# Kernel optimization log

Measured on AMD Instinct MI355X. Metric: run time of the kernel, lower is better.

## Reference

```python
import jax, jax.numpy as jnp
import numpy as np

D_MODEL = 512
D_K = 64
D_V = 128
H = D_MODEL // D_V  # 4 heads (num_head = d_model // d_v per the source)
B, N = 4, 2048


def setup_inputs() -> dict:
    key = jax.random.key(0)
    k0, k1, k2, k3, k4 = jax.random.split(key, 5)
    s = 0.02
    return {
        "input_x": jax.random.normal(k0, (B, N, D_MODEL), jnp.float32),
        "Wq": jax.random.normal(k1, (D_MODEL, H * D_K), jnp.float32) * s,
        "Wk": jax.random.normal(k2, (D_MODEL, H * D_K), jnp.float32) * s,
        "Wv": jax.random.normal(k3, (D_MODEL, D_MODEL), jnp.float32) * s,
        "Wo": jax.random.normal(k4, (D_MODEL, D_MODEL), jnp.float32) * s,
    }


def reference(input_x, Wq, Wk, Wv, Wo):
    b, n, _ = input_x.shape
    # Contiguous per-head slices in the source == a simple reshape here.
    q = (input_x @ Wq).reshape(b, n, H, D_K)   # [B,N,H,dk]
    k = (input_x @ Wk).reshape(b, n, H, D_K)   # [B,N,H,dk]
    v = (input_x @ Wv).reshape(b, n, H, D_V)   # [B,N,H,dv]
    scale = jnp.sqrt(jnp.float32(D_K))
    scores = jnp.einsum('bqhd,bkhd->bhqk', q, k) / scale  # [B,H,N,N]
    # FAITHFUL quirk: the source uses nn.Softmax() with no dim on a 3D
    # (B,N,N) tensor; PyTorch's legacy dim inference picks dim=0 (batch).
    attn = jax.nn.softmax(scores, axis=0)
    out = jnp.einsum('bhqk,bkhd->bqhd', attn, v).reshape(b, n, H * D_V)
    return out @ Wo
```

## Files before the change

kernel.cpp:

```cpp
#include <hip/hip_runtime.h>
#include <hip/hip_bf16.h>


typedef __attribute__((ext_vector_type(8))) short short8;
typedef __attribute__((ext_vector_type(4))) float floatx4;
typedef unsigned short u16;
typedef unsigned int u32;

#define MFMA16(a, b, c) __builtin_amdgcn_mfma_f32_16x16x32_bf16((a), (b), (c), 0, 0, 0)

__device__ __forceinline__ u16 f2bf(float f) {
    union { float f; unsigned u; } v; v.f = f;
    unsigned r = v.u + 0x7fffu + ((v.u >> 16) & 1u);
    return (u16)(r >> 16);
}

__device__ __forceinline__ float bf2f(u16 b) {
    union { unsigned u; float f; } v; v.u = ((u32)b) << 16;
    return v.f;
}

__device__ __forceinline__ u32 pk2bf(float a, float b) {
#if __has_builtin(__builtin_amdgcn_cvt_pk_bf16_f32)
    typedef __attribute__((ext_vector_type(2))) __bf16 bf16x2;
    union { bf16x2 v; u32 u; } c;
    c.v = __builtin_amdgcn_cvt_pk_bf16_f32(a, b);
    return c.u;
#else
    return (u32)f2bf(a) | ((u32)f2bf(b) << 16);
#endif
}

__device__ __forceinline__ float ex2(float x) {
#if __has_builtin(__builtin_amdgcn_exp2f)
    return __builtin_amdgcn_exp2f(x);
#else
    return exp2f(x);
#endif
}

__device__ __forceinline__ void gload_lds16(const u16* g, u16* l) {
    __builtin_amdgcn_global_load_lds(
        (const __attribute__((address_space(1))) void*)(const void*)g,
        (__attribute__((address_space(3))) void*)(void*)l, 16, 0, 0);
}

__global__ __launch_bounds__(256) void prep_all_kernel(
    const float* __restrict__ x, u16* __restrict__ xb,
    const float* __restrict__ Wq, const float* __restrict__ Wk,
    const float* __restrict__ Wv, const float* __restrict__ Wo,
    u16* __restrict__ WallT, u16* __restrict__ WoT) {
    int bid = blockIdx.x;
    if (bid < 4096) {
        int i = bid * 256 + threadIdx.x;
        float4 v = ((const float4*)x)[i];
        ushort4 o;
        o.x = f2bf(v.x); o.y = f2bf(v.y); o.z = f2bf(v.z); o.w = f2bf(v.w);
        ((ushort4*)xb)[i] = o;
        return;
    }
    int i = (bid - 4096) * 256 + threadIdx.x;
    if (i < 524288) {
        int n = i >> 9, k = i & 511;
        float v;
        if (n < 256)      v = Wq[k * 256 + n] * 0.18033688011f;
        else if (n < 512) v = Wk[k * 256 + (n - 256)];
        else              v = Wv[k * 512 + (n - 512)];
        WallT[i] = f2bf(v);
    } else {
        int j = i - 524288;
        int n = j >> 9, k = j & 511;
        WoT[j] = f2bf(Wo[k * 512 + n]);
    }
}

__global__ __launch_bounds__(512) void gemm_qkv_kernel(
    const u16* __restrict__ A, const u16* __restrict__ BT,
    u16* __restrict__ Qp, u16* __restrict__ Kp, u16* __restrict__ Vp,
    int Kdim) {
    __shared__ u16 sm[16896];
    u16* Asl = sm;
    u16* Bsl = sm + 8192;
    const int tid = threadIdx.x;
    const int bid0 = blockIdx.y * 8 + blockIdx.x;
    const int xcd = bid0 & 7, jj = bid0 >> 3;
    const int mbase = (xcd * 8 + (jj >> 3)) * 128;
    const int nbase = (jj & 7) * 128;
    const int wave = tid >> 6, lane = tid & 63;
    const int wm = wave >> 2, wn = wave & 3;
    const int lq = lane & 15, quad = lane >> 4;

    const u16* gA = A + (size_t)(mbase + wave * 16 + (lane >> 3)) * Kdim + (lane & 7) * 8;
    const u16* gB = BT + (size_t)(nbase + wave * 16 + (lane >> 3)) * Kdim + (lane & 7) * 8;
    u16* lA = &Asl[(wave * 16) * 64];
    u16* lB = &Bsl[(wave * 16) * 64];

    const floatx4 z4 = {0.f, 0.f, 0.f, 0.f};
    floatx4 acc[4][2];
#pragma unroll
    for (int i = 0; i < 4; i++)
#pragma unroll
        for (int j = 0; j < 2; j++) acc[i][j] = z4;

    const int nk = Kdim >> 6;
    for (int kk = 0; kk < nk; kk++) {
        const int kb = kk << 6;
        if (kk) __syncthreads();
#pragma unroll
        for (int i = 0; i < 2; i++) {
            gload_lds16(gA + kb + (size_t)(i * 8) * Kdim, lA + (i * 8) * 64);
            gload_lds16(gB + kb + (size_t)(i * 8) * Kdim, lB + (i * 8) * 64);
        }
        __syncthreads();
#pragma unroll
        for (int ki = 0; ki < 2; ki++) {
            short8 af[4], bf[2];
#pragma unroll
            for (int mi = 0; mi < 4; mi++)
                af[mi] = *(const short8*)&Asl[(wm * 64 + mi * 16 + lq) * 64 + ki * 32 + quad * 8];
#pragma unroll
            for (int ni = 0; ni < 2; ni++)
                bf[ni] = *(const short8*)&Bsl[(wn * 32 + ni * 16 + lq) * 64 + ki * 32 + quad * 8];
#pragma unroll
            for (int mi = 0; mi < 4; mi++)
#pragma unroll
                for (int ni = 0; ni < 2; ni++)
                    acc[mi][ni] = MFMA16(af[mi], bf[ni], acc[mi][ni]);
        }
    }
    __syncthreads();
    const bool vtile = (nbase >= 512);
#pragma unroll
    for (int mi = 0; mi < 4; mi++)
#pragma unroll
        for (int ni = 0; ni < 2; ni++) {
            int cl = wn * 32 + ni * 16 + lq;
#pragma unroll
            for (int r = 0; r < 4; r++) {
                int rl = wm * 64 + mi * 16 + quad * 4 + r;
                if (vtile) sm[cl * 132 + rl] = f2bf(acc[mi][ni][r]);
                else       sm[rl * 132 + cl] = f2bf(acc[mi][ni][r]);
            }
        }
    __syncthreads();
    const int b = mbase >> 11;
    const int keyb = mbase & 2047;
    if (nbase < 256) {
        const int hq = nbase >> 6;
        const int qs_base = keyb >> 4;
#pragma unroll
        for (int t = 0; t < 4; t++) {
            int l = wave * 4 + t;
            int qs2 = l >> 2, h2 = (l >> 1) & 1, ki = l & 1;
            int qd = lane >> 4, lqq = lane & 15;
            short8 v = *(const short8*)&sm[(qs2 * 16 + lqq) * 132 + h2 * 64 + ki * 32 + qd * 8];
            int h = hq + h2;
            size_t base = ((size_t)(((b * 4 + h) * 128 + (qs_base + qs2)) * 2 + ki) * 64 + lane) << 3;
            *(short8*)&Qp[base] = v;
        }
    } else if (nbase < 512) {
        const int hb = (nbase - 256) >> 6;
        const int ktb = keyb >> 6;
#pragma unroll
        for (int t = 0; t < 4; t++) {
            int l = wave * 4 + t;
            int kt2 = l >> 4, hf = (l >> 3) & 1, nj = (l >> 2) & 1;
            int h2 = (l >> 1) & 1, ki = l & 1;
            int quadk = lane >> 4, lqk = lane & 15;
            short8 v = *(const short8*)&sm[(kt2 * 64 + hf * 32 + lqk * 2 + nj) * 132 +
                                           h2 * 64 + ki * 32 + quadk * 8];
            int h = hb + h2;
            size_t base = ((size_t)(((((b * 4 + h) * 32 + (ktb + kt2)) * 2 + hf) * 2 + nj)
                                    * 2 + ki) * 64 + lane) << 3;
            *(short8*)&Kp[base] = v;
        }
    } else {
        const int h = (nbase - 512) >> 7;
        const int ktb = keyb >> 6;
#pragma unroll
        for (int t = 0; t < 4; t++) {
            int l = wave * 4 + t;
            int kt2 = l >> 4, hf = (l >> 3) & 1, niv = (l >> 1) & 3, wv = l & 1;
            int quadv = lane >> 4, lqv = lane & 15;
            short8 v = *(const short8*)&sm[(hf * 64 + niv * 16 + lqv) * 132 +
                                           kt2 * 64 + wv * 32 + quadv * 8];
            size_t base = ((size_t)(((((b * 4 + h) * 32 + (ktb + kt2)) * 2 + hf) * 4 + niv)
                                    * 2 + wv) * 64 + lane) << 3;
            *(short8*)&Vp[base] = v;
        }
    }
}

__global__ __launch_bounds__(512) void gemm_out_kernel(
    const u16* __restrict__ A, const u16* __restrict__ BT,
    float* __restrict__ Cf, int Kdim, int ldc) {
    __shared__ u16 Asl[64 * 64];
    __shared__ u16 Bsl[128 * 64];
    const int tid = threadIdx.x;
    const int bid0 = blockIdx.y * 4 + blockIdx.x;
    const int xcd = bid0 & 7, jj = bid0 >> 3;
    const int mbase = (xcd * 16 + (jj >> 2)) * 64;
    const int nbase = (jj & 3) * 128;
    const int wave = tid >> 6, lane = tid & 63;
    const int wm = wave >> 2, wn = wave & 3;
    const int lq = lane & 15, quad = lane >> 4;
    const size_t S = (size_t)8192 * 512;

    const u16* gA = A + (size_t)(mbase + wave * 8 + (lane >> 3)) * Kdim + (lane & 7) * 8;
    const u16* gB = BT + (size_t)(nbase + wave * 16 + (lane >> 3)) * Kdim + (lane & 7) * 8;
    u16* lAw = &Asl[(wave * 8 + (lane >> 3)) * 64 + (lane & 7) * 8];
    u16* lB = &Bsl[(wave * 16) * 64];

    const floatx4 z4 = {0.f, 0.f, 0.f, 0.f};
    floatx4 acc[2][2];
#pragma unroll
    for (int i = 0; i < 2; i++)
#pragma unroll
        for (int j = 0; j < 2; j++) acc[i][j] = z4;

    const int nk = Kdim >> 6;
    for (int kk = 0; kk < nk; kk++) {
        const int kb = kk << 6;
        short8 p0 = *(const short8*)(gA + kb);
        short8 p1 = *(const short8*)(gA + kb + S);
        short8 p2 = *(const short8*)(gA + kb + 2 * S);
        short8 p3 = *(const short8*)(gA + kb + 3 * S);
        if (kk) __syncthreads();
        gload_lds16(gB + kb, lB);
        gload_lds16(gB + kb + (size_t)8 * Kdim, lB + 8 * 64);
        short8 o;
#pragma unroll
        for (int j2 = 0; j2 < 8; j2++) {
            float s = bf2f((u16)p0[j2]) + bf2f((u16)p1[j2]) +
                      bf2f((u16)p2[j2]) + bf2f((u16)p3[j2]);
            o[j2] = (short)f2bf(s);
        }
        *(short8*)lAw = o;
        __syncthreads();
#pragma unroll
        for (int ki = 0; ki < 2; ki++) {
            short8 af[2], bf[2];
#pragma unroll
            for (int mi = 0; mi < 2; mi++)
                af[mi] = *(const short8*)&Asl[(wm * 32 + mi * 16 + lq) * 64 + ki * 32 + quad * 8];
#pragma unroll
            for (int ni = 0; ni < 2; ni++)
                bf[ni] = *(const short8*)&Bsl[(wn * 32 + ni * 16 + lq) * 64 + ki * 32 + quad * 8];
#pragma unroll
            for (int mi = 0; mi < 2; mi++)
#pragma unroll
                for (int ni = 0; ni < 2; ni++)
                    acc[mi][ni] = MFMA16(af[mi], bf[ni], acc[mi][ni]);
        }
    }
#pragma unroll
    for (int mi = 0; mi < 2; mi++)
#pragma unroll
        for (int ni = 0; ni < 2; ni++)
#pragma unroll
            for (int r = 0; r < 4; r++)
                Cf[(size_t)(mbase + wm * 32 + mi * 16 + quad * 4 + r) * ldc +
                   (nbase + wn * 32 + ni * 16 + lq)] = acc[mi][ni][r];
}

__global__ __launch_bounds__(512) void attn_kernel(const u16* __restrict__ Qp,
                                                   const u16* __restrict__ Kp,
                                                   const u16* __restrict__ Vp,
                                                   u16* __restrict__ Pp) {
    __shared__ u16 pl[2 * 4 * 4096];
    const int bx = blockIdx.x;
    const int xcd = bx & 7;
    const int j8 = bx >> 3;
    const int sl = xcd * 2 + (j8 >> 5);
    const int h = sl & 3;
    const int ck = sl >> 2;
    const int qt = j8 & 31;
    const int tid = threadIdx.x;
    const int wave = tid >> 6, lane = tid & 63;
    const int mi = wave & 3, half = wave >> 2;
    const int dq = wave;
    const int half_v = dq >> 2, ni_v = dq & 3;
    const int lq = lane & 15, quad = lane >> 4;
    const int qs = qt * 4 + mi;

    short8 aq[4][2];
#pragma unroll
    for (int b = 0; b < 4; b++)
#pragma unroll
        for (int ki = 0; ki < 2; ki++)
            aq[b][ki] = *(const short8*)&Qp[
                ((size_t)((((b * 4 + h) * 128 + qs) * 2 + ki) * 64 + lane) << 3)];

    const floatx4 z4 = {0.f, 0.f, 0.f, 0.f};
    floatx4 oacc[4][4];
#pragma unroll
    for (int b = 0; b < 4; b++)
#pragma unroll
        for (int m2 = 0; m2 < 4; m2++) oacc[b][m2] = z4;

    for (int kt = ck * 8; kt < ck * 8 + 8; kt++) {
        u16* plb = &pl[((kt & 1) * 4 + mi) * 4096];
        u16* plbuf = &pl[(kt & 1) * 4 * 4096];
        floatx4 s[4][2];
        __builtin_amdgcn_s_setprio(1);
#pragma unroll
        for (int b = 0; b < 4; b++) {
            const u16* kb = Kp +
                ((size_t)((((b * 4 + h) * 32 + kt) * 2 + half) * 2) << 10) +
                lane * 8;
#pragma unroll
            for (int nj = 0; nj < 2; nj++) {
                s[b][nj] = z4;
#pragma unroll
                for (int ki = 0; ki < 2; ki++)
                    s[b][nj] = MFMA16(aq[b][ki],
                                      *(const short8*)(kb + (nj * 2 + ki) * 512),
                                      s[b][nj]);
            }
        }
        __builtin_amdgcn_s_setprio(0);
        short8 vf[4][2];
#pragma unroll
        for (int b = 0; b < 4; b++) {
            const u16* vb = Vp +
                ((size_t)(((((b * 4 + h) * 32 + kt) * 2 + half_v) * 4 + ni_v) * 2) << 9) +
                lane * 8;
            vf[b][0] = *(const short8*)vb;
            vf[b][1] = *(const short8*)(vb + 512);
        }
#pragma unroll
        for (int r = 0; r < 4; r++) {
            float e0a = ex2(s[0][0][r]), e0b = ex2(s[0][1][r]);
            float e1a = ex2(s[1][0][r]), e1b = ex2(s[1][1][r]);
            float e2a = ex2(s[2][0][r]), e2b = ex2(s[2][1][r]);
            float e3a = ex2(s[3][0][r]), e3b = ex2(s[3][1][r]);
            float ia = __builtin_amdgcn_rcpf(e0a + e1a + e2a + e3a);
            float ib = __builtin_amdgcn_rcpf(e0b + e1b + e2b + e3b);
            int q = quad * 4 + r;
            int col = (half * 32 + 2 * lq) ^ ((q & 7) * 8);
            *(u32*)&plb[(0 * 16 + q) * 64 + col] = pk2bf(e0a * ia, e0b * ib);
            *(u32*)&plb[(1 * 16 + q) * 64 + col] = pk2bf(e1a * ia, e1b * ib);
            *(u32*)&plb[(2 * 16 + q) * 64 + col] = pk2bf(e2a * ia, e2b * ib);
            *(u32*)&plb[(3 * 16 + q) * 64 + col] = pk2bf(e3a * ia, e3b * ib);
        }
        __syncthreads();
        const int sw = (lq & 7) * 8;
        __builtin_amdgcn_s_setprio(1);
#pragma unroll
        for (int b = 0; b < 4; b++) {
#pragma unroll
            for (int m2 = 0; m2 < 4; m2++) {
                const u16* pm = plbuf + m2 * 4096;
                short8 ap0 = *(const short8*)&pm[(b * 16 + lq) * 64 + ((quad * 8) ^ sw)];
                short8 ap1 = *(const short8*)&pm[(b * 16 + lq) * 64 + ((32 + quad * 8) ^ sw)];
                oacc[b][m2] = MFMA16(ap0, vf[b][0], oacc[b][m2]);
                oacc[b][m2] = MFMA16(ap1, vf[b][1], oacc[b][m2]);
            }
        }
        __builtin_amdgcn_s_setprio(0);
    }
    u16* Pc = Pp + (size_t)ck * (8192 * 512);
#pragma unroll
    for (int b = 0; b < 4; b++)
#pragma unroll
        for (int m2 = 0; m2 < 4; m2++)
#pragma unroll
            for (int r = 0; r < 4; r++)
                Pc[(size_t)(b * 2048 + qt * 64 + m2 * 16 + quad * 4 + r) * 512 +
                   h * 128 + dq * 16 + lq] = f2bf(oacc[b][m2][r]);
}

extern "C" void kernel_launch(void* const* d_in, const int* in_sizes, int n_in,
                              void* d_out, int out_size, void* d_ws, size_t ws_size,
                              hipStream_t stream) {
    const float* x  = (const float*)d_in[0];
    const float* Wq = (const float*)d_in[1];
    const float* Wk = (const float*)d_in[2];
    const float* Wv = (const float*)d_in[3];
    const float* Wo = (const float*)d_in[4];
    float* out = (float*)d_out;

    char* ws = (char*)d_ws;
    u16* Pp    = (u16*)ws;
    u16* Xb    = (u16*)ws;
    u16* WallT = (u16*)(ws + (size_t)8 * 1024 * 1024);
    char* tail = ws + (size_t)32 * 1024 * 1024;
    u16* WoT   = (u16*)tail; tail += (size_t)512 * 512 * 2;
    u16* Qp    = (u16*)tail; tail += (size_t)8192 * 256 * 2;
    u16* Kp    = (u16*)tail; tail += (size_t)8192 * 256 * 2;
    u16* Vp    = (u16*)tail; tail += (size_t)8192 * 512 * 2;

    prep_all_kernel<<<7168, 256, 0, stream>>>(x, Xb, Wq, Wk, Wv, Wo, WallT, WoT);
    gemm_qkv_kernel<<<dim3(8, 64), 512, 0, stream>>>(Xb, WallT, Qp, Kp, Vp, 512);
    attn_kernel<<<512, 512, 0, stream>>>(Qp, Kp, Vp, Pp);
    gemm_out_kernel<<<dim3(4, 128), 512, 0, stream>>>(Pp, WoT, out, 512, 512);
}
```

Before: 165.5 us.

## Prefetch next K tile for two batches and simplify block index mapping

Loads the K fragments for batches 0 and 1 of the next key tile into registers during the P·V phase of the current iteration, so the QK^T MFMAs for those batches do not wait on global loads. The block index decoding drops the XCD-aware swizzle in favour of a plain linear mapping of head, chunk and query tile. The s_setprio hints around the MFMA sections are also removed. Prefetching raises register pressure, and the new mapping can change L2 locality across XCDs.

```diff
diff --git a/kernel.cpp b/kernel.cpp
--- a/kernel.cpp
+++ b/kernel.cpp
@@ -269,12 +269,9 @@
                                                    u16* __restrict__ Pp) {
     __shared__ u16 pl[2 * 4 * 4096];
     const int bx = blockIdx.x;
-    const int xcd = bx & 7;
-    const int j8 = bx >> 3;
-    const int sl = xcd * 2 + (j8 >> 5);
-    const int h = sl & 3;
-    const int ck = sl >> 2;
-    const int qt = j8 & 31;
+    const int h = bx & 3;
+    const int ck = (bx >> 2) & 3;
+    const int qt = bx >> 4;
     const int tid = threadIdx.x;
     const int wave = tid >> 6, lane = tid & 63;
     const int mi = wave & 3, half = wave >> 2;
@@ -298,13 +295,30 @@
 #pragma unroll
         for (int m2 = 0; m2 < 4; m2++) oacc[b][m2] = z4;
 
+    short8 kf[2][4];
+#pragma unroll
+    for (int b = 0; b < 2; b++) {
+        const u16* kb = Kp +
+            ((size_t)((((b * 4 + h) * 32 + ck * 8) * 2 + half) * 2) << 10) + lane * 8;
+#pragma unroll
+        for (int f = 0; f < 4; f++) kf[b][f] = *(const short8*)(kb + f * 512);
+    }
+
     for (int kt = ck * 8; kt < ck * 8 + 8; kt++) {
         u16* plb = &pl[((kt & 1) * 4 + mi) * 4096];
         u16* plbuf = &pl[(kt & 1) * 4 * 4096];
         floatx4 s[4][2];
-        __builtin_amdgcn_s_setprio(1);
-#pragma unroll
-        for (int b = 0; b < 4; b++) {
+#pragma unroll
+        for (int b = 0; b < 2; b++)
+#pragma unroll
+            for (int nj = 0; nj < 2; nj++) {
+                s[b][nj] = z4;
+#pragma unroll
+                for (int ki = 0; ki < 2; ki++)
+                    s[b][nj] = MFMA16(aq[b][ki], kf[b][nj * 2 + ki], s[b][nj]);
+            }
+#pragma unroll
+        for (int b = 2; b < 4; b++) {
             const u16* kb = Kp +
                 ((size_t)((((b * 4 + h) * 32 + kt) * 2 + half) * 2) << 10) +
                 lane * 8;
@@ -318,7 +332,6 @@
                                       s[b][nj]);
             }
         }
-        __builtin_amdgcn_s_setprio(0);
         short8 vf[4][2];
 #pragma unroll
         for (int b = 0; b < 4; b++) {
@@ -344,8 +357,18 @@
             *(u32*)&plb[(3 * 16 + q) * 64 + col] = pk2bf(e3a * ia, e3b * ib);
         }
         __syncthreads();
+        {
+            int ktn = kt + 1; if (ktn > 31) ktn = 31;
+#pragma unroll
+            for (int b = 0; b < 2; b++) {
+                const u16* kb = Kp +
+                    ((size_t)((((b * 4 + h) * 32 + ktn) * 2 + half) * 2) << 10) +
+                    lane * 8;
+#pragma unroll
+                for (int f = 0; f < 4; f++) kf[b][f] = *(const short8*)(kb + f * 512);
+            }
+        }
         const int sw = (lq & 7) * 8;
-        __builtin_amdgcn_s_setprio(1);
 #pragma unroll
         for (int b = 0; b < 4; b++) {
 #pragma unroll
@@ -357,7 +380,6 @@
                 oacc[b][m2] = MFMA16(ap1, vf[b][1], oacc[b][m2]);
             }
         }
-        __builtin_amdgcn_s_setprio(0);
     }
     u16* Pc = Pp + (size_t)ck * (8192 * 512);
 #pragma unroll
```

Result: no change. 162.7 us (-1.7%).
